# Performance work log

Hardware: AMD Instinct MI355X
Metric: run time of the kernel (lower is better)

## Reference

```python
import jax, jax.numpy as jnp
import numpy as np

B, T, H, HEADS, K, L = 64, 512, 512, 4, 3, 16
R, A = 256, 9


def _pe(t, h):
    pos = np.arange(t)[:, None].astype(np.float32)
    div = np.exp(-np.log(10000.0) * np.arange(0, h, 2).astype(np.float32) / h)
    pe = np.zeros((t, h), np.float32)
    pe[:, 0::2] = np.sin(pos * div)
    pe[:, 1::2] = np.cos(pos * div)
    return jnp.asarray(pe)


def _ln(x, g, b, eps=1e-5):
    m = x.mean(-1, keepdims=True)
    v = ((x - m) ** 2).mean(-1, keepdims=True)
    return (x - m) * jax.lax.rsqrt(v + eps) * g + b


def _dwconv(x, k):
    # x [B,T,C], k [K,C]: depthwise temporal conv, SAME padding
    kern = k[:, None, :]  # [K, 1, C] in WIO layout, groups = C
    return jax.lax.conv_general_dilated(
        x, kern, (1,), 'SAME',
        dimension_numbers=('NWC', 'WIO', 'NWC'),
        feature_group_count=x.shape[-1])


def setup_inputs():
    key = jax.random.key(0)
    ks = jax.random.split(key, 16)
    n = lambda i, shape, s=0.02: jax.random.normal(ks[i], shape, jnp.float32) * s
    return dict(
        rssi=jax.random.normal(ks[0], (B, T, R), jnp.float32),
        accl=jax.random.normal(ks[1], (B, T, A), jnp.float32),
        rssi_W=n(2, (R, H)), rssi_b=jnp.zeros((H,), jnp.float32),
        accl_W=n(3, (A, H)), accl_b=jnp.zeros((H,), jnp.float32),
        conv_r=n(4, (K, H), 0.1), conv_a=n(5, (K, H), 0.1),
        Wq=n(6, (H, H)), Wk=n(7, (H, H)), Wv=n(8, (H, H)), Wo=n(9, (H, H)),
        ln1_g=jnp.ones((H,), jnp.float32), ln1_b=jnp.zeros((H,), jnp.float32),
        W1=n(10, (H, 4 * H)), b1=jnp.zeros((4 * H,), jnp.float32),
        W2=n(11, (4 * H, H)), b2=jnp.zeros((H,), jnp.float32),
        ln2_g=jnp.ones((H,), jnp.float32), ln2_b=jnp.zeros((H,), jnp.float32),
        loc_W=n(12, (H, L)), loc_b=jnp.zeros((L,), jnp.float32),
        start_trans=n(13, (L,), 0.1), end_trans=n(14, (L,), 0.1),
        trans=n(15, (L, L), 0.1),
    )


def _emissions(rssi, accl, rssi_W, rssi_b, accl_W, accl_b, conv_r, conv_a,
               Wq, Wk, Wv, Wo, ln1_g, ln1_b, W1, b1, W2, b2, ln2_g, ln2_b,
               loc_W, loc_b):
    t, h = rssi.shape[1], rssi_W.shape[1]
    pe = _pe(t, h)
    r = rssi @ rssi_W + rssi_b + pe                   # [B,T,H]
    a = accl @ accl_W + accl_b + pe                   # [B,T,H]
    x = _dwconv(r, conv_r) + _dwconv(a, conv_a)       # dual-conv fusion
    b_, t_, _ = x.shape
    dh = h // HEADS
    q = (x @ Wq).reshape(b_, t_, HEADS, dh)
    k = (x @ Wk).reshape(b_, t_, HEADS, dh)
    v = (x @ Wv).reshape(b_, t_, HEADS, dh)
    logits = jnp.einsum('bqhd,bkhd->bhqk', q, k) / jnp.sqrt(jnp.float32(dh))
    attn = jax.nn.softmax(logits, axis=-1)
    o = jnp.einsum('bhqk,bkhd->bqhd', attn, v).reshape(b_, t_, h) @ Wo
    x = _ln(x + o, ln1_g, ln1_b)
    f = jax.nn.relu(x @ W1 + b1) @ W2 + b2
    x = _ln(x + f, ln2_g, ln2_b)
    return x @ loc_W + loc_b                          # emissions [B,T,L]


def _viterbi(em, start_trans, end_trans, trans):
    # torchcrf-style Viterbi decode (batch_first, full-length sequences)
    score0 = start_trans + em[:, 0]                   # [B,L]

    def step(score, em_t):
        tot = score[:, :, None] + trans[None] + em_t[:, None, :]  # [B,L,L]
        return tot.max(axis=1), tot.argmax(axis=1)

    score, hist = jax.lax.scan(step, score0, jnp.swapaxes(em[:, 1:], 0, 1))
    final = score + end_trans
    last = jnp.argmax(final, axis=-1)                 # [B]
    best = jnp.max(final, axis=-1)                    # [B] best-path score

    def back(tag, h):
        prev = jnp.take_along_axis(h, tag[:, None], axis=1)[:, 0]
        return prev, prev

    _, path = jax.lax.scan(back, last, hist, reverse=True)
    tags = jnp.concatenate([path, last[None]], axis=0)  # [T,B]
    return jnp.swapaxes(tags, 0, 1).astype(jnp.int64), best


def reference(rssi, accl, rssi_W, rssi_b, accl_W, accl_b, conv_r, conv_a,
              Wq, Wk, Wv, Wo, ln1_g, ln1_b, W1, b1, W2, b2, ln2_g, ln2_b,
              loc_W, loc_b, start_trans, end_trans, trans):
    em = _emissions(rssi, accl, rssi_W, rssi_b, accl_W, accl_b, conv_r, conv_a,
                    Wq, Wk, Wv, Wo, ln1_g, ln1_b, W1, b1, W2, b2,
                    ln2_g, ln2_b, loc_W, loc_b)
    tags, _ = _viterbi(em, start_trans, end_trans, trans)
    return tags  # [B,T] int decoded locations
```

## Files before the change

### kernel.cpp

```cpp
#include <hip/hip_runtime.h>
#include <math.h>

constexpr int Bc = 64, Tc = 512, Hc = 512, HEADSc = 4, Lc = 16, Rc = 256, Ac = 9;
constexpr int DH = 128;

#define F_BIAS 1
#define F_PE   2
#define F_ADDC 4
#define F_RELU 8
#define F_DIV  16
#define F_QKV  32

using short8   = __attribute__((ext_vector_type(8)))  short;
using floatx16 = __attribute__((ext_vector_type(16))) float;
using ushort4v = __attribute__((ext_vector_type(4)))  unsigned short;

struct S3 { unsigned short h, m, l; };
__device__ inline S3 split3(float v)
{
    S3 r;
    unsigned u = __float_as_uint(v);
    r.h = (unsigned short)(u >> 16);
    float r1 = v - __uint_as_float(u & 0xffff0000u);
    unsigned u1 = __float_as_uint(r1);
    r.m = (unsigned short)(u1 >> 16);
    float r2 = r1 - __uint_as_float(u1 & 0xffff0000u);
    r.l = (unsigned short)(__float_as_uint(r2) >> 16);
    return r;
}

template<bool BSPLIT>
__global__ __launch_bounds__(256)
void mgemm(const float* __restrict__ A, const float* __restrict__ Bf,
           const unsigned short* __restrict__ Bsp, long long bPS,
           float* __restrict__ C, const float* __restrict__ bias,
           const float* __restrict__ pe,
           int M, int N, int K, int lda, int ldb, int ldc,
           long long s1A, long long s2A, long long s1B, long long s2B,
           long long s1C, long long s2C, float divv, int flags)
{
    int z = blockIdx.z, z1 = z >> 2, z2 = z & 3;
    A += (size_t)z1 * s1A + (size_t)z2 * s2A;
    if (!BSPLIT) Bf += (size_t)z1 * s1B + (size_t)z2 * s2B;
    C += (size_t)z1 * s1C + (size_t)z2 * s2C;

    __shared__ unsigned short Ah[128][40], Am[128][40], Al[128][40];
    __shared__ unsigned short Bh[128][40], Bm[128][40], Bl[128][40];

    int bm = blockIdx.y * 128, bn = blockIdx.x * 128;
    int tid = threadIdx.x;
    int lane = tid & 63, wave = tid >> 6;
    int wr = wave >> 1, wc = wave & 1;
    int l31 = lane & 31, khalf = lane >> 5;

    floatx16 acc[2][2];
    #pragma unroll
    for (int i = 0; i < 2; i++)
        #pragma unroll
        for (int j = 0; j < 2; j++)
            #pragma unroll
            for (int e = 0; e < 16; e++) acc[i][j][e] = 0.f;

    for (int k0 = 0; k0 < K; k0 += 32) {
        #pragma unroll
        for (int it = 0; it < 4; it++) {
            int s = tid + 256 * it;
            int mm = s >> 3, kc = (s & 7) << 2;
            float4 v = *(const float4*)(A + (size_t)(bm + mm) * lda + k0 + kc);
            ushort4v h, m, l;
            S3 s0 = split3(v.x); h[0] = s0.h; m[0] = s0.m; l[0] = s0.l;
            S3 s1 = split3(v.y); h[1] = s1.h; m[1] = s1.m; l[1] = s1.l;
            S3 s2 = split3(v.z); h[2] = s2.h; m[2] = s2.m; l[2] = s2.l;
            S3 s3 = split3(v.w); h[3] = s3.h; m[3] = s3.m; l[3] = s3.l;
            *(ushort4v*)&Ah[mm][kc] = h;
            *(ushort4v*)&Am[mm][kc] = m;
            *(ushort4v*)&Al[mm][kc] = l;
        }
        if (BSPLIT) {
            #pragma unroll
            for (int it = 0; it < 2; it++) {
                int s = tid + 256 * it;
                int nn = s >> 2, kc = (s & 3) << 3;
                size_t go = (size_t)(bn + nn) * ldb + k0 + kc;
                *(short8*)&Bh[nn][kc] = *(const short8*)(Bsp + go);
                *(short8*)&Bm[nn][kc] = *(const short8*)(Bsp + bPS + go);
                *(short8*)&Bl[nn][kc] = *(const short8*)(Bsp + 2 * bPS + go);
            }
        } else {
            #pragma unroll
            for (int it = 0; it < 4; it++) {
                int s = tid + 256 * it;
                int nn = s >> 3, kc = (s & 7) << 2;
                float4 v = *(const float4*)(Bf + (size_t)(bn + nn) * ldb + k0 + kc);
                ushort4v h, m, l;
                S3 s0 = split3(v.x); h[0] = s0.h; m[0] = s0.m; l[0] = s0.l;
                S3 s1 = split3(v.y); h[1] = s1.h; m[1] = s1.m; l[1] = s1.l;
                S3 s2 = split3(v.z); h[2] = s2.h; m[2] = s2.m; l[2] = s2.l;
                S3 s3 = split3(v.w); h[3] = s3.h; m[3] = s3.m; l[3] = s3.l;
                *(ushort4v*)&Bh[nn][kc] = h;
                *(ushort4v*)&Bm[nn][kc] = m;
                *(ushort4v*)&Bl[nn][kc] = l;
            }
        }
        __syncthreads();

        #pragma unroll
        for (int s = 0; s < 2; s++) {
            int ko = s * 16 + khalf * 8;
            short8 a0[2], a1[2], a2[2], b0[2], b1[2], b2[2];
            #pragma unroll
            for (int i = 0; i < 2; i++) {
                int ar = wr * 64 + i * 32 + l31;
                a0[i] = *(const short8*)&Ah[ar][ko];
                a1[i] = *(const short8*)&Am[ar][ko];
                a2[i] = *(const short8*)&Al[ar][ko];
                int br = wc * 64 + i * 32 + l31;
                b0[i] = *(const short8*)&Bh[br][ko];
                b1[i] = *(const short8*)&Bm[br][ko];
                b2[i] = *(const short8*)&Bl[br][ko];
            }
            #pragma unroll
            for (int i = 0; i < 2; i++)
                #pragma unroll
                for (int j = 0; j < 2; j++)
                    acc[i][j] = __builtin_amdgcn_mfma_f32_32x32x16_bf16(a0[i], b0[j], acc[i][j], 0, 0, 0);
            #pragma unroll
            for (int i = 0; i < 2; i++)
                #pragma unroll
                for (int j = 0; j < 2; j++)
                    acc[i][j] = __builtin_amdgcn_mfma_f32_32x32x16_bf16(a0[i], b1[j], acc[i][j], 0, 0, 0);
            #pragma unroll
            for (int i = 0; i < 2; i++)
                #pragma unroll
                for (int j = 0; j < 2; j++)
                    acc[i][j] = __builtin_amdgcn_mfma_f32_32x32x16_bf16(a1[i], b0[j], acc[i][j], 0, 0, 0);
            #pragma unroll
            for (int i = 0; i < 2; i++)
                #pragma unroll
                for (int j = 0; j < 2; j++)
                    acc[i][j] = __builtin_amdgcn_mfma_f32_32x32x16_bf16(a0[i], b2[j], acc[i][j], 0, 0, 0);
            #pragma unroll
            for (int i = 0; i < 2; i++)
                #pragma unroll
                for (int j = 0; j < 2; j++)
                    acc[i][j] = __builtin_amdgcn_mfma_f32_32x32x16_bf16(a2[i], b0[j], acc[i][j], 0, 0, 0);
            #pragma unroll
            for (int i = 0; i < 2; i++)
                #pragma unroll
                for (int j = 0; j < 2; j++)
                    acc[i][j] = __builtin_amdgcn_mfma_f32_32x32x16_bf16(a1[i], b1[j], acc[i][j], 0, 0, 0);
        }
        __syncthreads();
    }

    #pragma unroll
    for (int i = 0; i < 2; i++) {
        #pragma unroll
        for (int j = 0; j < 2; j++) {
            #pragma unroll
            for (int r = 0; r < 16; r++) {
                int m = bm + wr * 64 + i * 32 + (r & 3) + ((r >> 2) << 3) + (khalf << 2);
                int n = bn + wc * 64 + j * 32 + l31;
                float v = acc[i][j][r];
                if (flags & F_DIV)  v /= divv;
                if (flags & F_BIAS) v += bias[n];
                if (flags & F_PE)   v += pe[(size_t)(m & (Tc - 1)) * Hc + n];
                if (flags & F_QKV) {
                    long long gth = s1C;
                    if (n < 512) {
                        C[(size_t)m * 512 + n] = v;
                    } else if (n < 1024) {
                        C[gth + (size_t)m * 512 + (n - 512)] = v;
                    } else {
                        C[2 * gth + (size_t)(m >> 9) * (Tc * Hc)
                          + (size_t)(n - 1024) * Tc + (m & (Tc - 1))] = v;
                    }
                } else {
                    if (flags & F_ADDC) v += C[(size_t)m * ldc + n];
                    if (flags & F_RELU) v = fmaxf(v, 0.f);
                    C[(size_t)m * ldc + n] = v;
                }
            }
        }
    }
}

__global__ __launch_bounds__(256)
void wsplit_kernel(const float* __restrict__ W, unsigned short* __restrict__ out,
                   int K, int N, long long PS)
{
    __shared__ float t[64][65];
    int k0 = blockIdx.x * 64, n0 = blockIdx.y * 64;
    int tid = threadIdx.x;
    int c = tid & 63, r4 = tid >> 6;
    #pragma unroll
    for (int i = 0; i < 16; i++) {
        int r = r4 * 16 + i;
        t[r][c] = W[(size_t)(k0 + r) * N + n0 + c];
    }
    __syncthreads();
    #pragma unroll
    for (int i = 0; i < 16; i++) {
        int n = r4 * 16 + i;
        S3 s = split3(t[c][n]);
        size_t o = (size_t)(n0 + n) * K + k0 + c;
        out[o] = s.h; out[PS + o] = s.m; out[2 * PS + o] = s.l;
    }
}

__global__ void pe_kernel(float* __restrict__ pe)
{
    int idx = blockIdx.x * 256 + threadIdx.x;
    if (idx >= Tc * Hc) return;
    int t = idx >> 9, n = idx & (Hc - 1);
    int j = n >> 1;
    double div = exp(-log(10000.0) * (double)(2 * j) / (double)Hc);
    double arg = (double)t * div;
    pe[idx] = (float)((n & 1) ? cos(arg) : sin(arg));
}

__global__ __launch_bounds__(256)
void accl_kernel(const float* __restrict__ accl, const float* __restrict__ W,
                 const float* __restrict__ bias, const float* __restrict__ pe,
                 float* __restrict__ out)
{
    int idx = blockIdx.x * 256 + threadIdx.x;
    int n = idx & (Hc - 1);
    int m = idx >> 9;
    int t = m & (Tc - 1);
    const float* arow = accl + (size_t)m * Ac;
    float s = 0.f;
    #pragma unroll
    for (int i = 0; i < Ac; i++) s += arow[i] * W[i * Hc + n];
    s += bias[n];
    s += pe[t * Hc + n];
    out[idx] = s;
}

__global__ __launch_bounds__(256)
void dwconv_kernel(const float* __restrict__ r, const float* __restrict__ a,
                   const float* __restrict__ cr, const float* __restrict__ ca,
                   float* __restrict__ x)
{
    int idx = blockIdx.x * 256 + threadIdx.x;
    int c = idx & (Hc - 1);
    int m = idx >> 9;
    int t = m & (Tc - 1);
    float vr = r[idx] * cr[Hc + c];
    if (t > 0)      vr = r[idx - Hc] * cr[c] + vr;
    if (t < Tc - 1) vr = vr + r[idx + Hc] * cr[2 * Hc + c];
    float va = a[idx] * ca[Hc + c];
    if (t > 0)      va = a[idx - Hc] * ca[c] + va;
    if (t < Tc - 1) va = va + a[idx + Hc] * ca[2 * Hc + c];
    x[idx] = vr + va;
}

__global__ __launch_bounds__(256)
void softmax_kernel(float* __restrict__ L)
{
    size_t base = (size_t)blockIdx.x * 512;
    int tid = threadIdx.x;
    float v0 = L[base + tid], v1 = L[base + tid + 256];
    __shared__ float buf[256];
    buf[tid] = fmaxf(v0, v1);
    __syncthreads();
    for (int s = 128; s > 0; s >>= 1) {
        if (tid < s) buf[tid] = fmaxf(buf[tid], buf[tid + s]);
        __syncthreads();
    }
    float mx = buf[0];
    __syncthreads();
    float e0 = expf(v0 - mx), e1 = expf(v1 - mx);
    buf[tid] = e0 + e1;
    __syncthreads();
    for (int s = 128; s > 0; s >>= 1) {
        if (tid < s) buf[tid] += buf[tid + s];
        __syncthreads();
    }
    float sum = buf[0];
    L[base + tid] = e0 / sum;
    L[base + tid + 256] = e1 / sum;
}

__global__ __launch_bounds__(256)
void add_ln_kernel(const float* __restrict__ X, const float* __restrict__ Y,
                   const float* __restrict__ g, const float* __restrict__ bta,
                   float* __restrict__ out)
{
    size_t base = (size_t)blockIdx.x * 512;
    int tid = threadIdx.x;
    float v0 = X[base + tid] + Y[base + tid];
    float v1 = X[base + tid + 256] + Y[base + tid + 256];
    __shared__ float buf[256];
    buf[tid] = v0 + v1;
    __syncthreads();
    for (int s = 128; s > 0; s >>= 1) {
        if (tid < s) buf[tid] += buf[tid + s];
        __syncthreads();
    }
    float mean = buf[0] / 512.f;
    __syncthreads();
    float d0 = v0 - mean, d1 = v1 - mean;
    buf[tid] = d0 * d0 + d1 * d1;
    __syncthreads();
    for (int s = 128; s > 0; s >>= 1) {
        if (tid < s) buf[tid] += buf[tid + s];
        __syncthreads();
    }
    float var = buf[0] / 512.f;
    float rs = 1.0f / sqrtf(var + 1e-5f);
    out[base + tid]       = d0 * rs * g[tid] + bta[tid];
    out[base + tid + 256] = d1 * rs * g[tid + 256] + bta[tid + 256];
}

__global__ __launch_bounds__(256)
void em_kernel(const float* __restrict__ X, const float* __restrict__ W,
               const float* __restrict__ bias, float* __restrict__ out)
{
    __shared__ float Wl[8192];
    int tid = threadIdx.x;
    #pragma unroll
    for (int i = 0; i < 32; i++) Wl[tid + 256 * i] = W[tid + 256 * i];
    __syncthreads();
    int r = tid >> 4, l = tid & 15;
    const float* xr = X + ((size_t)blockIdx.x * 16 + r) * Hc;
    float s = 0.f;
    #pragma unroll 8
    for (int k = 0; k < Hc; k++) s += xr[k] * Wl[k * Lc + l];
    s += bias[l];
    out[((size_t)blockIdx.x * 16 + r) * Lc + l] = s;
}

__global__ __launch_bounds__(64)
void viterbi_kernel(const float* __restrict__ em, const float* __restrict__ st,
                    const float* __restrict__ et, const float* __restrict__ trans,
                    int* __restrict__ out)
{
    int b = blockIdx.x;
    int tid = threadIdx.x;
    __shared__ float ems[2][64][Lc];
    __shared__ float sc[2][Lc];
    __shared__ unsigned char hist[Tc - 1][Lc];
    float trcol[Lc];
    if (tid < Lc) {
        #pragma unroll
        for (int i = 0; i < Lc; i++) trcol[i] = trans[i * Lc + tid];
    }
    const float* emb = em + (size_t)b * Tc * Lc;
    {
        const float4* src = (const float4*)emb;
        float4* dst = (float4*)&ems[0][0][0];
        #pragma unroll
        for (int i = 0; i < 4; i++) dst[tid + 64 * i] = src[tid + 64 * i];
    }
    __syncthreads();
    if (tid < Lc) sc[0][tid] = st[tid] + ems[0][0][tid];
    __syncthreads();
    int cur = 0;
    for (int c = 0; c < 8; c++) {
        if (c < 7) {
            const float4* src = (const float4*)(emb + (size_t)(c + 1) * 64 * Lc);
            float4* dst = (float4*)&ems[(c + 1) & 1][0][0];
            #pragma unroll
            for (int i = 0; i < 4; i++) dst[tid + 64 * i] = src[tid + 64 * i];
        }
        int tt0 = (c == 0) ? 1 : 0;
        for (int tt = tt0; tt < 64; tt++) {
            int t = c * 64 + tt;
            if (tid < Lc) {
                float e = ems[c & 1][tt][tid];
                float v[Lc];
                #pragma unroll
                for (int i = 0; i < Lc; i++) v[i] = (sc[cur][i] + trcol[i]) + e;
                float bv[8]; int bi[8];
                #pragma unroll
                for (int i = 0; i < 8; i++) {
                    bool ge = v[2 * i] >= v[2 * i + 1];
                    bv[i] = ge ? v[2 * i] : v[2 * i + 1];
                    bi[i] = ge ? 2 * i : 2 * i + 1;
                }
                #pragma unroll
                for (int i = 0; i < 4; i++) {
                    bool ge = bv[2 * i] >= bv[2 * i + 1];
                    bv[i] = ge ? bv[2 * i] : bv[2 * i + 1];
                    bi[i] = ge ? bi[2 * i] : bi[2 * i + 1];
                }
                #pragma unroll
                for (int i = 0; i < 2; i++) {
                    bool ge = bv[2 * i] >= bv[2 * i + 1];
                    bv[i] = ge ? bv[2 * i] : bv[2 * i + 1];
                    bi[i] = ge ? bi[2 * i] : bi[2 * i + 1];
                }
                bool ge = bv[0] >= bv[1];
                sc[cur ^ 1][tid] = ge ? bv[0] : bv[1];
                hist[t - 1][tid] = (unsigned char)(ge ? bi[0] : bi[1]);
            }
            __syncthreads();
            cur ^= 1;
        }
    }
    if (tid == 0) {
        float best = sc[cur][0] + et[0];
        int tag = 0;
        #pragma unroll
        for (int j = 1; j < Lc; j++) {
            float v = sc[cur][j] + et[j];
            if (v > best) { best = v; tag = j; }
        }
        out[(size_t)b * Tc + (Tc - 1)] = tag;
        for (int t = Tc - 2; t >= 0; t--) {
            tag = hist[t][tag];
            out[(size_t)b * Tc + t] = tag;
        }
    }
}

__global__ void diag_kernel(int* __restrict__ out, int n, int val)
{
    int i = blockIdx.x * 256 + threadIdx.x;
    if (i < n) out[i] = val;
}

extern "C" void kernel_launch(void* const* d_in, const int* in_sizes, int n_in,
                              void* d_out, int out_size, void* d_ws, size_t ws_size,
                              hipStream_t stream)
{
    const float* rssi   = (const float*)d_in[0];
    const float* accl   = (const float*)d_in[1];
    const float* rssi_W = (const float*)d_in[2];
    const float* rssi_b = (const float*)d_in[3];
    const float* accl_W = (const float*)d_in[4];
    const float* accl_b = (const float*)d_in[5];
    const float* conv_r = (const float*)d_in[6];
    const float* conv_a = (const float*)d_in[7];
    const float* Wq     = (const float*)d_in[8];
    const float* Wk     = (const float*)d_in[9];
    const float* Wv     = (const float*)d_in[10];
    const float* Wo     = (const float*)d_in[11];
    const float* ln1_g  = (const float*)d_in[12];
    const float* ln1_b  = (const float*)d_in[13];
    const float* W1     = (const float*)d_in[14];
    const float* b1     = (const float*)d_in[15];
    const float* W2     = (const float*)d_in[16];
    const float* b2     = (const float*)d_in[17];
    const float* ln2_g  = (const float*)d_in[18];
    const float* ln2_b  = (const float*)d_in[19];
    const float* loc_W  = (const float*)d_in[20];
    const float* loc_b  = (const float*)d_in[21];
    const float* start_trans = (const float*)d_in[22];
    const float* end_trans   = (const float*)d_in[23];
    const float* trans       = (const float*)d_in[24];

    const int M = Bc * Tc;
    const size_t S = (size_t)M * Hc;
    const size_t TH = (size_t)Tc * Hc;
    const long long TT = (long long)Tc * Tc;
    const float sq = sqrtf((float)DH);
    dim3 blk(256);

    const size_t WBUF_SH = 9830400ull;
    const size_t WBUF_F  = WBUF_SH / 2;
    size_t total_f = ws_size / sizeof(float);
    size_t work_min = (size_t)M * 128;
    if (total_f < 2 * S + WBUF_F + TH + work_min) {
        diag_kernel<<<dim3((out_size + 255) / 256), blk, 0, stream>>>(
            (int*)d_out, out_size, 1000000 + (int)(ws_size >> 20));
        return;
    }

    float* bufX = (float*)d_ws;
    float* bufY = bufX + S;
    unsigned short* wbuf  = (unsigned short*)(bufY + S);
    unsigned short* rssiT = wbuf;
    unsigned short* qkvT  = wbuf + 393216;
    unsigned short* WoT   = wbuf + 2752512;
    unsigned short* W1T   = wbuf + 3538944;
    unsigned short* W2T   = wbuf + 6684672;
    float* pe_buf = (float*)(wbuf + WBUF_SH);
    float* work = pe_buf + TH;
    size_t work_n = total_f - 2 * S - WBUF_F - TH;

    int Ge = 1;
    for (int g = 64; g >= 1; g >>= 1) if ((size_t)g * TH <= work_n) { Ge = g; break; }
    int Ga = 1;
    for (int g = 64; g >= 1; g >>= 1) if (8ull * g * TH <= work_n) { Ga = g; break; }
    int Nc = 128;
    for (int n = 2048; n >= 128; n >>= 1) if ((size_t)M * n <= work_n) { Nc = n; break; }

    pe_kernel<<<dim3((Tc * Hc + 255) / 256), blk, 0, stream>>>(pe_buf);
    wsplit_kernel<<<dim3(Rc / 64, Hc / 64), blk, 0, stream>>>(rssi_W, rssiT, Rc, Hc, 131072LL);
    wsplit_kernel<<<dim3(8, 8),  blk, 0, stream>>>(Wq, qkvT,          512, 512, 786432LL);
    wsplit_kernel<<<dim3(8, 8),  blk, 0, stream>>>(Wk, qkvT + 262144, 512, 512, 786432LL);
    wsplit_kernel<<<dim3(8, 8),  blk, 0, stream>>>(Wv, qkvT + 524288, 512, 512, 786432LL);
    wsplit_kernel<<<dim3(8, 8),  blk, 0, stream>>>(Wo, WoT, 512, 512, 262144LL);
    wsplit_kernel<<<dim3(8, 32), blk, 0, stream>>>(W1, W1T, 512, 2048, 1048576LL);
    wsplit_kernel<<<dim3(32, 8), blk, 0, stream>>>(W2, W2T, 2048, 512, 1048576LL);

    accl_kernel<<<dim3(M * (Hc / 256)), blk, 0, stream>>>(accl, accl_W, accl_b, pe_buf, bufY);
    for (int g0 = 0; g0 < Bc; g0 += Ge) {
        int rows = Ge * Tc;
        mgemm<true><<<dim3(Hc / 128, rows / 128, 1), blk, 0, stream>>>(
            rssi + (size_t)g0 * Tc * Rc, nullptr, rssiT, 131072LL,
            work, rssi_b, pe_buf,
            rows, Hc, Rc, Rc, Rc, Hc,
            0, 0, 0, 0, 0, 0, 1.f, F_BIAS | F_PE);
        dwconv_kernel<<<dim3(rows * (Hc / 256)), blk, 0, stream>>>(
            work, bufY + (size_t)g0 * TH, conv_r, conv_a, bufX + (size_t)g0 * TH);
    }

    for (int g0 = 0; g0 < Bc; g0 += Ga) {
        int rows = Ga * Tc;
        long long gth = (long long)Ga * TH;
        float* qg = work;
        float* kg = work + gth;
        float* vg = work + 2 * gth;
        float* og = work + 3 * gth;
        float* lg = work + 4 * gth;
        mgemm<true><<<dim3(1536 / 128, rows / 128, 1), blk, 0, stream>>>(
            bufX + (size_t)g0 * TH, nullptr, qkvT, 786432LL,
            qg, nullptr, nullptr,
            rows, 1536, Hc, Hc, 512, 0,
            0, 0, 0, 0, gth, 0, 1.f, F_QKV);
        mgemm<false><<<dim3(Tc / 128, Tc / 128, Ga * HEADSc), blk, 0, stream>>>(
            qg, kg, nullptr, 0,
            lg, nullptr, nullptr,
            Tc, Tc, DH, Hc, Hc, Tc,
            (long long)TH, DH, (long long)TH, DH,
            (long long)HEADSc * TT, TT, sq, F_DIV);
        softmax_kernel<<<dim3(Ga * HEADSc * Tc), blk, 0, stream>>>(lg);
        mgemm<false><<<dim3(DH / 128, Tc / 128, Ga * HEADSc), blk, 0, stream>>>(
            lg, vg, nullptr, 0,
            og, nullptr, nullptr,
            Tc, DH, Tc, Tc, Tc, Hc,
            (long long)HEADSc * TT, TT,
            (long long)TH, (long long)DH * Tc,
            (long long)TH, DH, 1.f, 0);
        mgemm<true><<<dim3(Hc / 128, rows / 128, 1), blk, 0, stream>>>(
            og, nullptr, WoT, 262144LL,
            bufY + (size_t)g0 * TH, nullptr, nullptr,
            rows, Hc, Hc, Hc, 512, Hc,
            0, 0, 0, 0, 0, 0, 1.f, 0);
    }

    add_ln_kernel<<<dim3(M), blk, 0, stream>>>(bufX, bufY, ln1_g, ln1_b, bufX);

    int nChunks = 2048 / Nc;
    for (int c = 0; c < nChunks; c++) {
        mgemm<true><<<dim3(Nc / 128, M / 128, 1), blk, 0, stream>>>(
            bufX, nullptr, W1T + (size_t)c * Nc * 512, 1048576LL,
            work, b1 + c * Nc, nullptr,
            M, Nc, Hc, Hc, 512, Nc,
            0, 0, 0, 0, 0, 0, 1.f, F_BIAS | F_RELU);
        mgemm<true><<<dim3(Hc / 128, M / 128, 1), blk, 0, stream>>>(
            work, nullptr, W2T + (size_t)c * Nc, 1048576LL,
            bufY, b2, nullptr,
            M, Hc, Nc, Nc, 2048, Hc,
            0, 0, 0, 0, 0, 0, 1.f, (c == 0) ? F_BIAS : F_ADDC);
    }

    add_ln_kernel<<<dim3(M), blk, 0, stream>>>(bufX, bufY, ln2_g, ln2_b, bufX);

    em_kernel<<<dim3(M / 16), blk, 0, stream>>>(bufX, loc_W, loc_b, work);

    viterbi_kernel<<<dim3(Bc), dim3(64), 0, stream>>>(
        work, start_trans, end_trans, trans, (int*)d_out);
}
```

Before: 3.247 ms.

## Pre-split activations to bf16x3, fuse accl projection into dwconv, shuffle-based Viterbi

Adds an asplit kernel that splits activations into three bf16 planes once, so the QKV and W1 GEMMs load pre-split A tiles instead of re-splitting fp32 per output-column tile. Folds the tiny accl projection into the depthwise conv kernel, which recomputes it for each of the three taps and no longer writes an intermediate buffer. Rewrites the Viterbi forward pass to use all 64 lanes with wave shuffles and packed (score, index) max, dropping the per-step __syncthreads. This costs extra workspace, which changes the Ga/Nc chunk sizing, plus extra split passes over the activations.

```diff
diff --git a/kernel.cpp b/kernel.cpp
--- a/kernel.cpp
+++ b/kernel.cpp
@@ -29,10 +29,12 @@
     return r;
 }
 
-template<bool BSPLIT>
+template<bool ASP, bool BSP>
 __global__ __launch_bounds__(256)
-void mgemm(const float* __restrict__ A, const float* __restrict__ Bf,
-           const unsigned short* __restrict__ Bsp, long long bPS,
+void mgemm(const float* __restrict__ Af, const unsigned short* __restrict__ Asp,
+           long long aPS,
+           const float* __restrict__ Bf, const unsigned short* __restrict__ Bsp,
+           long long bPS,
            float* __restrict__ C, const float* __restrict__ bias,
            const float* __restrict__ pe,
            int M, int N, int K, int lda, int ldb, int ldc,
@@ -40,12 +42,14 @@
            long long s1C, long long s2C, float divv, int flags)
 {
     int z = blockIdx.z, z1 = z >> 2, z2 = z & 3;
-    A += (size_t)z1 * s1A + (size_t)z2 * s2A;
-    if (!BSPLIT) Bf += (size_t)z1 * s1B + (size_t)z2 * s2B;
-    C += (size_t)z1 * s1C + (size_t)z2 * s2C;
-
-    __shared__ unsigned short Ah[128][40], Am[128][40], Al[128][40];
-    __shared__ unsigned short Bh[128][40], Bm[128][40], Bl[128][40];
+    if (ASP) Asp += (size_t)z1 * s1A + (size_t)z2 * s2A;
+    else     Af  += (size_t)z1 * s1A + (size_t)z2 * s2A;
+    if (BSP) Bsp += (size_t)z1 * s1B + (size_t)z2 * s2B;
+    else     Bf  += (size_t)z1 * s1B + (size_t)z2 * s2B;
+    if (!(flags & F_QKV)) C += (size_t)z1 * s1C + (size_t)z2 * s2C;
+
+    __shared__ unsigned short As[3][128][40];
+    __shared__ unsigned short Bs[3][128][40];
 
     int bm = blockIdx.y * 128, bn = blockIdx.x * 128;
     int tid = threadIdx.x;
@@ -62,29 +66,41 @@
             for (int e = 0; e < 16; e++) acc[i][j][e] = 0.f;
 
     for (int k0 = 0; k0 < K; k0 += 32) {
-        #pragma unroll
-        for (int it = 0; it < 4; it++) {
-            int s = tid + 256 * it;
-            int mm = s >> 3, kc = (s & 7) << 2;
-            float4 v = *(const float4*)(A + (size_t)(bm + mm) * lda + k0 + kc);
-            ushort4v h, m, l;
-            S3 s0 = split3(v.x); h[0] = s0.h; m[0] = s0.m; l[0] = s0.l;
-            S3 s1 = split3(v.y); h[1] = s1.h; m[1] = s1.m; l[1] = s1.l;
-            S3 s2 = split3(v.z); h[2] = s2.h; m[2] = s2.m; l[2] = s2.l;
-            S3 s3 = split3(v.w); h[3] = s3.h; m[3] = s3.m; l[3] = s3.l;
-            *(ushort4v*)&Ah[mm][kc] = h;
-            *(ushort4v*)&Am[mm][kc] = m;
-            *(ushort4v*)&Al[mm][kc] = l;
-        }
-        if (BSPLIT) {
+        if (ASP) {
+            #pragma unroll
+            for (int it = 0; it < 2; it++) {
+                int s = tid + 256 * it;
+                int rr = s >> 2, kc = (s & 3) << 3;
+                size_t ga = (size_t)(bm + rr) * lda + k0 + kc;
+                *(short8*)&As[0][rr][kc] = *(const short8*)(Asp + ga);
+                *(short8*)&As[1][rr][kc] = *(const short8*)(Asp + aPS + ga);
+                *(short8*)&As[2][rr][kc] = *(const short8*)(Asp + 2 * aPS + ga);
+            }
+        } else {
+            #pragma unroll
+            for (int it = 0; it < 4; it++) {
+                int s = tid + 256 * it;
+                int mm = s >> 3, kc = (s & 7) << 2;
+                float4 v = *(const float4*)(Af + (size_t)(bm + mm) * lda + k0 + kc);
+                ushort4v h, m, l;
+                S3 s0 = split3(v.x); h[0] = s0.h; m[0] = s0.m; l[0] = s0.l;
+                S3 s1 = split3(v.y); h[1] = s1.h; m[1] = s1.m; l[1] = s1.l;
+                S3 s2 = split3(v.z); h[2] = s2.h; m[2] = s2.m; l[2] = s2.l;
+                S3 s3 = split3(v.w); h[3] = s3.h; m[3] = s3.m; l[3] = s3.l;
+                *(ushort4v*)&As[0][mm][kc] = h;
+                *(ushort4v*)&As[1][mm][kc] = m;
+                *(ushort4v*)&As[2][mm][kc] = l;
+            }
+        }
+        if (BSP) {
             #pragma unroll
             for (int it = 0; it < 2; it++) {
                 int s = tid + 256 * it;
                 int nn = s >> 2, kc = (s & 3) << 3;
                 size_t go = (size_t)(bn + nn) * ldb + k0 + kc;
-                *(short8*)&Bh[nn][kc] = *(const short8*)(Bsp + go);
-                *(short8*)&Bm[nn][kc] = *(const short8*)(Bsp + bPS + go);
-                *(short8*)&Bl[nn][kc] = *(const short8*)(Bsp + 2 * bPS + go);
+                *(short8*)&Bs[0][nn][kc] = *(const short8*)(Bsp + go);
+                *(short8*)&Bs[1][nn][kc] = *(const short8*)(Bsp + bPS + go);
+                *(short8*)&Bs[2][nn][kc] = *(const short8*)(Bsp + 2 * bPS + go);
             }
         } else {
             #pragma unroll
@@ -97,9 +113,9 @@
                 S3 s1 = split3(v.y); h[1] = s1.h; m[1] = s1.m; l[1] = s1.l;
                 S3 s2 = split3(v.z); h[2] = s2.h; m[2] = s2.m; l[2] = s2.l;
                 S3 s3 = split3(v.w); h[3] = s3.h; m[3] = s3.m; l[3] = s3.l;
-                *(ushort4v*)&Bh[nn][kc] = h;
-                *(ushort4v*)&Bm[nn][kc] = m;
-                *(ushort4v*)&Bl[nn][kc] = l;
+                *(ushort4v*)&Bs[0][nn][kc] = h;
+                *(ushort4v*)&Bs[1][nn][kc] = m;
+                *(ushort4v*)&Bs[2][nn][kc] = l;
             }
         }
         __syncthreads();
@@ -111,13 +127,13 @@
             #pragma unroll
             for (int i = 0; i < 2; i++) {
                 int ar = wr * 64 + i * 32 + l31;
-                a0[i] = *(const short8*)&Ah[ar][ko];
-                a1[i] = *(const short8*)&Am[ar][ko];
-                a2[i] = *(const short8*)&Al[ar][ko];
+                a0[i] = *(const short8*)&As[0][ar][ko];
+                a1[i] = *(const short8*)&As[1][ar][ko];
+                a2[i] = *(const short8*)&As[2][ar][ko];
                 int br = wc * 64 + i * 32 + l31;
-                b0[i] = *(const short8*)&Bh[br][ko];
-                b1[i] = *(const short8*)&Bm[br][ko];
-                b2[i] = *(const short8*)&Bl[br][ko];
+                b0[i] = *(const short8*)&Bs[0][br][ko];
+                b1[i] = *(const short8*)&Bs[1][br][ko];
+                b2[i] = *(const short8*)&Bs[2][br][ko];
             }
             #pragma unroll
             for (int i = 0; i < 2; i++)
@@ -186,6 +202,26 @@
 }
 
 __global__ __launch_bounds__(256)
+void asplit_kernel(const float* __restrict__ X, unsigned short* __restrict__ out,
+                   long long PS, long long E)
+{
+    long long off = ((long long)blockIdx.x * 256 + threadIdx.x) * 8;
+    if (off >= E) return;
+    float4 v0 = *(const float4*)(X + off);
+    float4 v1 = *(const float4*)(X + off + 4);
+    short8 h, m, l;
+    float vv[8] = {v0.x, v0.y, v0.z, v0.w, v1.x, v1.y, v1.z, v1.w};
+    #pragma unroll
+    for (int i = 0; i < 8; i++) {
+        S3 s = split3(vv[i]);
+        h[i] = (short)s.h; m[i] = (short)s.m; l[i] = (short)s.l;
+    }
+    *(short8*)(out + off) = h;
+    *(short8*)(out + PS + off) = m;
+    *(short8*)(out + 2 * PS + off) = l;
+}
+
+__global__ __launch_bounds__(256)
 void wsplit_kernel(const float* __restrict__ W, unsigned short* __restrict__ out,
                    int K, int N, long long PS)
 {
@@ -220,38 +256,40 @@
 }
 
 __global__ __launch_bounds__(256)
-void accl_kernel(const float* __restrict__ accl, const float* __restrict__ W,
-                 const float* __restrict__ bias, const float* __restrict__ pe,
-                 float* __restrict__ out)
-{
-    int idx = blockIdx.x * 256 + threadIdx.x;
-    int n = idx & (Hc - 1);
-    int m = idx >> 9;
-    int t = m & (Tc - 1);
-    const float* arow = accl + (size_t)m * Ac;
-    float s = 0.f;
-    #pragma unroll
-    for (int i = 0; i < Ac; i++) s += arow[i] * W[i * Hc + n];
-    s += bias[n];
-    s += pe[t * Hc + n];
-    out[idx] = s;
-}
-
-__global__ __launch_bounds__(256)
-void dwconv_kernel(const float* __restrict__ r, const float* __restrict__ a,
-                   const float* __restrict__ cr, const float* __restrict__ ca,
-                   float* __restrict__ x)
+void dwconv_fused_kernel(const float* __restrict__ r,
+                         const float* __restrict__ accl,
+                         const float* __restrict__ aW, const float* __restrict__ ab,
+                         const float* __restrict__ pe,
+                         const float* __restrict__ cr, const float* __restrict__ ca,
+                         float* __restrict__ x)
 {
     int idx = blockIdx.x * 256 + threadIdx.x;
     int c = idx & (Hc - 1);
     int m = idx >> 9;
     int t = m & (Tc - 1);
+    float w[Ac];
+    #pragma unroll
+    for (int i = 0; i < Ac; i++) w[i] = aW[i * Hc + c];
+    float bb = ab[c];
+
+    auto aval = [&](int mm, int tt) {
+        const float* row = accl + (size_t)mm * Ac;
+        float s = 0.f;
+        #pragma unroll
+        for (int i = 0; i < Ac; i++) s += row[i] * w[i];
+        return s + bb + pe[tt * Hc + c];
+    };
+
     float vr = r[idx] * cr[Hc + c];
-    if (t > 0)      vr = r[idx - Hc] * cr[c] + vr;
-    if (t < Tc - 1) vr = vr + r[idx + Hc] * cr[2 * Hc + c];
-    float va = a[idx] * ca[Hc + c];
-    if (t > 0)      va = a[idx - Hc] * ca[c] + va;
-    if (t < Tc - 1) va = va + a[idx + Hc] * ca[2 * Hc + c];
+    float va = aval(m, t) * ca[Hc + c];
+    if (t > 0) {
+        vr = r[idx - Hc] * cr[c] + vr;
+        va = aval(m - 1, t - 1) * ca[c] + va;
+    }
+    if (t < Tc - 1) {
+        vr = vr + r[idx + Hc] * cr[2 * Hc + c];
+        va = va + aval(m + 1, t + 1) * ca[2 * Hc + c];
+    }
     x[idx] = vr + va;
 }
 
@@ -331,6 +369,19 @@
     out[((size_t)blockIdx.x * 16 + r) * Lc + l] = s;
 }
 
+__device__ inline unsigned long long vit_pack(float v, int idx)
+{
+    unsigned u = __float_as_uint(v);
+    unsigned ou = (u & 0x80000000u) ? ~u : (u | 0x80000000u);
+    return ((unsigned long long)ou << 8) | (unsigned)idx;
+}
+__device__ inline float vit_unpack(unsigned long long p)
+{
+    unsigned ou = (unsigned)(p >> 8);
+    unsigned u = (ou & 0x80000000u) ? (ou & 0x7fffffffu) : ~ou;
+    return __uint_as_float(u);
+}
+
 __global__ __launch_bounds__(64)
 void viterbi_kernel(const float* __restrict__ em, const float* __restrict__ st,
                     const float* __restrict__ et, const float* __restrict__ trans,
@@ -338,14 +389,13 @@
 {
     int b = blockIdx.x;
     int tid = threadIdx.x;
+    int j = tid & 15, q = tid >> 4;
     __shared__ float ems[2][64][Lc];
-    __shared__ float sc[2][Lc];
     __shared__ unsigned char hist[Tc - 1][Lc];
-    float trcol[Lc];
-    if (tid < Lc) {
-        #pragma unroll
-        for (int i = 0; i < Lc; i++) trcol[i] = trans[i * Lc + tid];
-    }
+    float tr0 = trans[(4 * q + 0) * Lc + j];
+    float tr1 = trans[(4 * q + 1) * Lc + j];
+    float tr2 = trans[(4 * q + 2) * Lc + j];
+    float tr3 = trans[(4 * q + 3) * Lc + j];
     const float* emb = em + (size_t)b * Tc * Lc;
     {
         const float4* src = (const float4*)emb;
@@ -354,9 +404,7 @@
         for (int i = 0; i < 4; i++) dst[tid + 64 * i] = src[tid + 64 * i];
     }
     __syncthreads();
-    if (tid < Lc) sc[0][tid] = st[tid] + ems[0][0][tid];
-    __syncthreads();
-    int cur = 0;
+    float sc = st[j] + ems[0][0][j];
     for (int c = 0; c < 8; c++) {
         if (c < 7) {
             const float4* src = (const float4*)(emb + (size_t)(c + 1) * 64 * Lc);
@@ -367,46 +415,37 @@
         int tt0 = (c == 0) ? 1 : 0;
         for (int tt = tt0; tt < 64; tt++) {
             int t = c * 64 + tt;
-            if (tid < Lc) {
-                float e = ems[c & 1][tt][tid];
-                float v[Lc];
-                #pragma unroll
-                for (int i = 0; i < Lc; i++) v[i] = (sc[cur][i] + trcol[i]) + e;
-                float bv[8]; int bi[8];
-                #pragma unroll
-                for (int i = 0; i < 8; i++) {
-                    bool ge = v[2 * i] >= v[2 * i + 1];
-                    bv[i] = ge ? v[2 * i] : v[2 * i + 1];
-                    bi[i] = ge ? 2 * i : 2 * i + 1;
-                }
-                #pragma unroll
-                for (int i = 0; i < 4; i++) {
-                    bool ge = bv[2 * i] >= bv[2 * i + 1];
-                    bv[i] = ge ? bv[2 * i] : bv[2 * i + 1];
-                    bi[i] = ge ? bi[2 * i] : bi[2 * i + 1];
-                }
-                #pragma unroll
-                for (int i = 0; i < 2; i++) {
-                    bool ge = bv[2 * i] >= bv[2 * i + 1];
-                    bv[i] = ge ? bv[2 * i] : bv[2 * i + 1];
-                    bi[i] = ge ? bi[2 * i] : bi[2 * i + 1];
-                }
-                bool ge = bv[0] >= bv[1];
-                sc[cur ^ 1][tid] = ge ? bv[0] : bv[1];
-                hist[t - 1][tid] = (unsigned char)(ge ? bi[0] : bi[1]);
-            }
-            __syncthreads();
-            cur ^= 1;
-        }
-    }
+            float e = ems[c & 1][tt][j];
+            float s0 = __shfl(sc, 4 * q + 0);
+            float s1 = __shfl(sc, 4 * q + 1);
+            float s2 = __shfl(sc, 4 * q + 2);
+            float s3 = __shfl(sc, 4 * q + 3);
+            unsigned long long p = vit_pack((s0 + tr0) + e, 15 - (4 * q + 0));
+            unsigned long long p1 = vit_pack((s1 + tr1) + e, 15 - (4 * q + 1));
+            unsigned long long p2 = vit_pack((s2 + tr2) + e, 15 - (4 * q + 2));
+            unsigned long long p3 = vit_pack((s3 + tr3) + e, 15 - (4 * q + 3));
+            if (p1 > p) p = p1;
+            if (p2 > p) p = p2;
+            if (p3 > p) p = p3;
+            unsigned long long po = __shfl_xor(p, 16);
+            if (po > p) p = po;
+            po = __shfl_xor(p, 32);
+            if (po > p) p = po;
+            sc = vit_unpack(p);
+            if (q == 0) hist[t - 1][j] = (unsigned char)(15 - (int)(p & 0xFF));
+        }
+        __syncthreads();
+    }
+    float fv = sc + et[j];
+    float bv = __shfl(fv, 0);
+    int tag = 0;
+    #pragma unroll
+    for (int i = 1; i < Lc; i++) {
+        float v = __shfl(fv, i);
+        if (v > bv) { bv = v; tag = i; }
+    }
+    __syncthreads();
     if (tid == 0) {
-        float best = sc[cur][0] + et[0];
-        int tag = 0;
-        #pragma unroll
-        for (int j = 1; j < Lc; j++) {
-            float v = sc[cur][j] + et[j];
-            if (v > best) { best = v; tag = j; }
-        }
         out[(size_t)b * Tc + (Tc - 1)] = tag;
         for (int t = Tc - 2; t >= 0; t--) {
             tag = hist[t][tag];
@@ -461,8 +500,7 @@
     const size_t WBUF_SH = 9830400ull;
     const size_t WBUF_F  = WBUF_SH / 2;
     size_t total_f = ws_size / sizeof(float);
-    size_t work_min = (size_t)M * 128;
-    if (total_f < 2 * S + WBUF_F + TH + work_min) {
+    if (total_f < 2 * S + WBUF_F + TH + (size_t)M * 128) {
         diag_kernel<<<dim3((out_size + 255) / 256), blk, 0, stream>>>(
             (int*)d_out, out_size, 1000000 + (int)(ws_size >> 20));
         return;
@@ -483,9 +521,16 @@
     int Ge = 1;
     for (int g = 64; g >= 1; g >>= 1) if ((size_t)g * TH <= work_n) { Ge = g; break; }
     int Ga = 1;
-    for (int g = 64; g >= 1; g >>= 1) if (8ull * g * TH <= work_n) { Ga = g; break; }
+    for (int g = 64; g >= 1; g >>= 1)
+        if ((19ull * g * TH) / 2 <= work_n) { Ga = g; break; }
+    const size_t X1S_F = 25165824ull;
+    bool ASP1 = (work_n >= X1S_F + (size_t)M * 128);
     int Nc = 128;
-    for (int n = 2048; n >= 128; n >>= 1) if ((size_t)M * n <= work_n) { Nc = n; break; }
+    {
+        size_t base = ASP1 ? X1S_F : 0;
+        for (int n = 2048; n >= 128; n >>= 1)
+            if (base + (size_t)M * n <= work_n) { Nc = n; break; }
+    }
 
     pe_kernel<<<dim3((Tc * Hc + 255) / 256), blk, 0, stream>>>(pe_buf);
     wsplit_kernel<<<dim3(Rc / 64, Hc / 64), blk, 0, stream>>>(rssi_W, rssiT, Rc, Hc, 131072LL);
@@ -496,47 +541,53 @@
     wsplit_kernel<<<dim3(8, 32), blk, 0, stream>>>(W1, W1T, 512, 2048, 1048576LL);
     wsplit_kernel<<<dim3(32, 8), blk, 0, stream>>>(W2, W2T, 2048, 512, 1048576LL);
 
-    accl_kernel<<<dim3(M * (Hc / 256)), blk, 0, stream>>>(accl, accl_W, accl_b, pe_buf, bufY);
     for (int g0 = 0; g0 < Bc; g0 += Ge) {
         int rows = Ge * Tc;
-        mgemm<true><<<dim3(Hc / 128, rows / 128, 1), blk, 0, stream>>>(
-            rssi + (size_t)g0 * Tc * Rc, nullptr, rssiT, 131072LL,
+        mgemm<false, true><<<dim3(Hc / 128, rows / 128, 1), blk, 0, stream>>>(
+            rssi + (size_t)g0 * Tc * Rc, nullptr, 0,
+            nullptr, rssiT, 131072LL,
             work, rssi_b, pe_buf,
             rows, Hc, Rc, Rc, Rc, Hc,
             0, 0, 0, 0, 0, 0, 1.f, F_BIAS | F_PE);
-        dwconv_kernel<<<dim3(rows * (Hc / 256)), blk, 0, stream>>>(
-            work, bufY + (size_t)g0 * TH, conv_r, conv_a, bufX + (size_t)g0 * TH);
+        dwconv_fused_kernel<<<dim3(rows * (Hc / 256)), blk, 0, stream>>>(
+            work, accl + (size_t)g0 * Tc * Ac, accl_W, accl_b, pe_buf,
+            conv_r, conv_a, bufX + (size_t)g0 * TH);
     }
 
     for (int g0 = 0; g0 < Bc; g0 += Ga) {
-        int rows = Ga * Tc;
-        long long gth = (long long)Ga * TH;
+        int g = Ga;
+        int rows = g * Tc;
+        long long gth = (long long)g * TH;
         float* qg = work;
         float* kg = work + gth;
-        float* vg = work + 2 * gth;
+        float* vT = work + 2 * gth;
         float* og = work + 3 * gth;
         float* lg = work + 4 * gth;
-        mgemm<true><<<dim3(1536 / 128, rows / 128, 1), blk, 0, stream>>>(
-            bufX + (size_t)g0 * TH, nullptr, qkvT, 786432LL,
+        unsigned short* xsS = (unsigned short*)(work + 8 * gth);
+        asplit_kernel<<<dim3((unsigned)(gth / 2048)), blk, 0, stream>>>(
+            bufX + (size_t)g0 * TH, xsS, gth, gth);
+        mgemm<true, true><<<dim3(12, rows / 128, 1), blk, 0, stream>>>(
+            nullptr, xsS, gth,
+            nullptr, qkvT, 786432LL,
             qg, nullptr, nullptr,
             rows, 1536, Hc, Hc, 512, 0,
             0, 0, 0, 0, gth, 0, 1.f, F_QKV);
-        mgemm<false><<<dim3(Tc / 128, Tc / 128, Ga * HEADSc), blk, 0, stream>>>(
-            qg, kg, nullptr, 0,
+        mgemm<false, false><<<dim3(Tc / 128, Tc / 128, g * HEADSc), blk, 0, stream>>>(
+            qg, nullptr, 0, kg, nullptr, 0,
             lg, nullptr, nullptr,
             Tc, Tc, DH, Hc, Hc, Tc,
             (long long)TH, DH, (long long)TH, DH,
             (long long)HEADSc * TT, TT, sq, F_DIV);
-        softmax_kernel<<<dim3(Ga * HEADSc * Tc), blk, 0, stream>>>(lg);
-        mgemm<false><<<dim3(DH / 128, Tc / 128, Ga * HEADSc), blk, 0, stream>>>(
-            lg, vg, nullptr, 0,
+        softmax_kernel<<<dim3(g * HEADSc * Tc), blk, 0, stream>>>(lg);
+        mgemm<false, false><<<dim3(1, Tc / 128, g * HEADSc), blk, 0, stream>>>(
+            lg, nullptr, 0, vT, nullptr, 0,
             og, nullptr, nullptr,
             Tc, DH, Tc, Tc, Tc, Hc,
             (long long)HEADSc * TT, TT,
             (long long)TH, (long long)DH * Tc,
             (long long)TH, DH, 1.f, 0);
-        mgemm<true><<<dim3(Hc / 128, rows / 128, 1), blk, 0, stream>>>(
-            og, nullptr, WoT, 262144LL,
+        mgemm<false, true><<<dim3(Hc / 128, rows / 128, 1), blk, 0, stream>>>(
+            og, nullptr, 0, nullptr, WoT, 262144LL,
             bufY + (size_t)g0 * TH, nullptr, nullptr,
             rows, Hc, Hc, Hc, 512, Hc,
             0, 0, 0, 0, 0, 0, 1.f, 0);
@@ -544,15 +595,32 @@
 
     add_ln_kernel<<<dim3(M), blk, 0, stream>>>(bufX, bufY, ln1_g, ln1_b, bufX);
 
+    unsigned short* x1S = (unsigned short*)work;
+    float* hbuf = work + (ASP1 ? X1S_F : 0);
+    if (ASP1) {
+        asplit_kernel<<<dim3(M * 512 / 2048), blk, 0, stream>>>(
+            bufX, x1S, (long long)M * 512, (long long)M * 512);
+    }
     int nChunks = 2048 / Nc;
     for (int c = 0; c < nChunks; c++) {
-        mgemm<true><<<dim3(Nc / 128, M / 128, 1), blk, 0, stream>>>(
-            bufX, nullptr, W1T + (size_t)c * Nc * 512, 1048576LL,
-            work, b1 + c * Nc, nullptr,
-            M, Nc, Hc, Hc, 512, Nc,
-            0, 0, 0, 0, 0, 0, 1.f, F_BIAS | F_RELU);
-        mgemm<true><<<dim3(Hc / 128, M / 128, 1), blk, 0, stream>>>(
-            work, nullptr, W2T + (size_t)c * Nc, 1048576LL,
+        if (ASP1) {
+            mgemm<true, true><<<dim3(Nc / 128, M / 128, 1), blk, 0, stream>>>(
+                nullptr, x1S, (long long)M * 512,
+                nullptr, W1T + (size_t)c * Nc * 512, 1048576LL,
+                hbuf, b1 + c * Nc, nullptr,
+                M, Nc, Hc, Hc, 512, Nc,
+                0, 0, 0, 0, 0, 0, 1.f, F_BIAS | F_RELU);
+        } else {
+            mgemm<false, true><<<dim3(Nc / 128, M / 128, 1), blk, 0, stream>>>(
+                bufX, nullptr, 0,
+                nullptr, W1T + (size_t)c * Nc * 512, 1048576LL,
+                hbuf, b1 + c * Nc, nullptr,
+                M, Nc, Hc, Hc, 512, Nc,
+                0, 0, 0, 0, 0, 0, 1.f, F_BIAS | F_RELU);
+        }
+        mgemm<false, true><<<dim3(Hc / 128, M / 128, 1), blk, 0, stream>>>(
+            hbuf, nullptr, 0,
+            nullptr, W2T + (size_t)c * Nc, 1048576LL,
             bufY, b2, nullptr,
             M, Hc, Nc, Nc, 2048, Hc,
             0, 0, 0, 0, 0, 0, 1.f, (c == 0) ? F_BIAS : F_ADDC);
```

After: 3.143 ms. -3.2%, faster.
